# Performance work log

Hardware: AMD Instinct MI355X
Metric: run time of the kernel (lower is better)

Reference implementation:

```python
import jax, jax.numpy as jnp
import numpy as np

LN_EPS = 1e-5
ATT_EPS = 1e-6

def layer_norm(x, scale, bias):
    mu = jnp.mean(x, axis=-1, keepdims=True)
    var = jnp.mean(jnp.square(x - mu), axis=-1, keepdims=True)
    return (x - mu) * jax.lax.rsqrt(var + LN_EPS) * scale + bias

def setup_inputs() -> dict:
    key = jax.random.key(0)
    ks = jax.random.split(key, 8)
    N, C, H = 16384, 1024, 8
    s = 0.02
    return {
        "x": jax.random.normal(ks[0], (N, C), dtype=jnp.float32),
        "Wq": jax.random.normal(ks[1], (C, C), dtype=jnp.float32) * s,
        "Wkv": jax.random.normal(ks[2], (C, 2 * C), dtype=jnp.float32) * s,
        "ln1_scale": jnp.ones((C,), dtype=jnp.float32),
        "ln1_bias": jnp.zeros((C,), dtype=jnp.float32),
        "W1": jax.random.normal(ks[3], (C, C), dtype=jnp.float32) * s,
        "b1": jnp.zeros((C,), dtype=jnp.float32),
        "W2": jax.random.normal(ks[4], (C, C), dtype=jnp.float32) * s,
        "b2": jnp.zeros((C,), dtype=jnp.float32),
        "ln2_scale": jnp.ones((C,), dtype=jnp.float32),
        "ln2_bias": jnp.zeros((C,), dtype=jnp.float32),
    }

def reference(x, Wq, Wkv, ln1_scale, ln1_bias, W1, b1, W2, b2, ln2_scale, ln2_bias):
    H = 8
    N, C = x.shape
    d = C // H
    # QKV projections; torch .view(-1, d, heads) splits last dim as (d, H)
    q = (x @ Wq).reshape(N, d, H)
    kv = x @ Wkv  # [N, 2C]
    k = kv[:, :C].reshape(N, d, H)
    v = kv[:, C:].reshape(N, d, H)
    # Kernelized linear attention per head (phi = elu + 1), global segment (bi=None)
    phi_q = jax.nn.elu(q) + 1.0
    phi_k = jax.nn.elu(k) + 1.0
    kv_sum = jnp.einsum('ndh,neh->deh', phi_k, v)      # [d, d, H]
    z = jnp.sum(phi_k, axis=0)                          # [d, H]
    num = jnp.einsum('ndh,deh->neh', phi_q, kv_sum)     # [N, d, H]
    den = jnp.einsum('ndh,dh->nh', phi_q, z)            # [N, H]
    t = (num / (den[:, None, :] + ATT_EPS)).reshape(N, C)
    # AddNorm (beta=False, dropout=0): ln(t + x)
    y = layer_norm(t + x, ln1_scale, ln1_bias)
    # FFN: Linear -> GELU (exact) -> Linear
    h = jax.nn.gelu(y @ W1 + b1, approximate=False)
    f = h @ W2 + b2
    return layer_norm(f + y, ln2_scale, ln2_bias)
```

## Files before the change

kernel.cpp:

```cpp
#include <hip/hip_runtime.h>
#include <hip/hip_bf16.h>
#include <cstdint>
#include <cstddef>

typedef __bf16 bf16_t;
typedef bf16_t bf16x4 __attribute__((ext_vector_type(4)));
typedef bf16_t bf16x8 __attribute__((ext_vector_type(8)));
typedef float f32x4 __attribute__((ext_vector_type(4)));

static constexpr int NROWS = 16384;
static constexpr int CDIM  = 1024;

__device__ __forceinline__ int p6(int k) {
  return (k & 32) | ((k & 12) << 1) | ((k & 16) >> 2) | (k & 3);
}
__device__ __forceinline__ int p6i(int s) {
  return (s & 32) | ((s & 4) << 2) | ((s & 24) >> 1) | (s & 3);
}
__device__ __forceinline__ int permc(int c) {
  return (c & ~63) | p6(c & 63);
}


__device__ __forceinline__ void gload16(const bf16_t* g, bf16_t* l) {
  __builtin_amdgcn_global_load_lds((const __attribute__((address_space(1))) void*)g,
                                   (__attribute__((address_space(3))) void*)l, 16, 0, 0);
}

__device__ __forceinline__ bf16x8 ldsf128(const bf16_t* lds, int row, int ldbytes, int kbyte) {
  const char* p = (const char*)lds + row * ldbytes + (kbyte ^ ((row & 7) << 4));
  return *(const bf16x8*)p;
}

__device__ __forceinline__ float phi_fn(float v) {
  return v > 0.f ? v + 1.f : expf(v);
}
__device__ __forceinline__ float gelu_fn(float v) {
  return 0.5f * v * (1.f + erff(v * 0.70710678118654752f));
}


__global__ void cast_x_kernel(const float* __restrict__ x, bf16_t* __restrict__ xb, long nchunks) {
  long i = (long)blockIdx.x * blockDim.x + threadIdx.x;
  long stride = (long)gridDim.x * blockDim.x;
  for (long c = i; c < nchunks; c += stride) {
    long row = c >> 7;
    int p0 = (int)(c & 127) << 3;
    int group = p0 & ~63;
    int ccl = (p0 >> 3) & 7;
    int klo = ((ccl & 4) << 3) | ((ccl & 3) << 2);
    const float* src = x + row * 1024 + group + klo;
    float4 a = *(const float4*)src;
    float4 b = *(const float4*)(src + 16);
    bf16x8 o;
    o[0] = (bf16_t)a.x; o[1] = (bf16_t)a.y; o[2] = (bf16_t)a.z; o[3] = (bf16_t)a.w;
    o[4] = (bf16_t)b.x; o[5] = (bf16_t)b.y; o[6] = (bf16_t)b.z; o[7] = (bf16_t)b.w;
    *(bf16x8*)(xb + row * 1024 + p0) = o;
  }
}

__global__ void prep_w_kernel(const float* __restrict__ Wq, const float* __restrict__ Wkv,
                              const float* __restrict__ W1, const float* __restrict__ W2,
                              bf16_t* __restrict__ wqkv_bt, bf16_t* __restrict__ w1bt,
                              bf16_t* __restrict__ w2bt) {
  __shared__ float tile[64][65];
  int mode = blockIdx.z;
  const float* src; int ld; bf16_t* dst; int permute;
  if (mode == 0)      { src = Wq;          ld = 1024; dst = wqkv_bt;                       permute = 1; }
  else if (mode == 1) { src = Wkv;         ld = 2048; dst = wqkv_bt + (size_t)1024 * 1024; permute = 1; }
  else if (mode == 2) { src = Wkv + 1024;  ld = 2048; dst = wqkv_bt + (size_t)2048 * 1024; permute = 1; }
  else if (mode == 3) { src = W1;          ld = 1024; dst = w1bt;                          permute = 0; }
  else                { src = W2;          ld = 1024; dst = w2bt;                          permute = 0; }
  int r0 = blockIdx.x * 64, c0 = blockIdx.y * 64;
  int tid = threadIdx.x;
#pragma unroll
  for (int i = 0; i < 16; i++) {
    int idx = i * 256 + tid; int rr = idx >> 6, cc = idx & 63;
    tile[rr][cc] = src[(size_t)(r0 + rr) * ld + c0 + cc];
  }
  __syncthreads();
#pragma unroll
  for (int i = 0; i < 16; i++) {
    int idx = i * 256 + tid; int cc = idx >> 6, rr = idx & 63;
    int c = c0 + cc;
    int a = permute ? (((c & 7) << 7) | (c >> 3)) : c;
    dst[(size_t)a * 1024 + r0 + p6(rr)] = (bf16_t)tile[rr][cc];
  }
}


template<int MODE>
__global__ __launch_bounds__(256, 4)
void gemm_bt_kernel(const bf16_t* __restrict__ A, const bf16_t* __restrict__ Bt,
                    const float* __restrict__ bias,
                    bf16_t* __restrict__ o0, bf16_t* __restrict__ o1, bf16_t* __restrict__ o2,
                    int M, int N, int K)
{
  __shared__ bf16_t As[128 * 64];
  __shared__ bf16_t Bs[128 * 64];
  const int tid  = threadIdx.x;
  const int lane = tid & 63;
  const int wave = tid >> 6;
  const int wr = (wave >> 1) * 64, wc = (wave & 1) * 64;
  const int l15 = lane & 15, g = lane >> 4;
  const int row0 = blockIdx.x * 128, col0 = blockIdx.y * 128;
  const int cb = wave * 256;
  f32x4 acc[4][4] = {};

  for (int kt = 0; kt < K; kt += 64) {
    __syncthreads();
#pragma unroll
    for (int it = 0; it < 4; ++it) {
      int ch = cb + it * 64 + lane;
      int r = ch >> 3;
      int csrc = (ch & 7) ^ (r & 7);
      gload16(A  + (size_t)(row0 + r) * K + kt + csrc * 8, As + (size_t)(cb + it * 64) * 8);
      gload16(Bt + (size_t)(col0 + r) * K + kt + csrc * 8, Bs + (size_t)(cb + it * 64) * 8);
    }
    __syncthreads();
#pragma unroll
    for (int ks = 0; ks < 2; ++ks) {
      bf16x8 af[4], bfr[4];
#pragma unroll
      for (int i = 0; i < 4; i++) af[i]  = ldsf128(As, wr + i * 16 + l15, 128, ks * 64 + 16 * g);
#pragma unroll
      for (int i = 0; i < 4; i++) bfr[i] = ldsf128(Bs, wc + i * 16 + l15, 128, ks * 64 + 16 * g);
#pragma unroll
      for (int i = 0; i < 4; i++)
#pragma unroll
        for (int j = 0; j < 4; j++)
          acc[i][j] = __builtin_amdgcn_mfma_f32_16x16x32_bf16(af[i], bfr[j], acc[i][j], 0, 0, 0);
    }
  }

#pragma unroll
  for (int i = 0; i < 4; i++) {
    int rbase = row0 + wr + i * 16 + g * 4;
#pragma unroll
    for (int j = 0; j < 4; j++) {
      int col = col0 + wc + j * 16 + l15;
      f32x4 v = acc[i][j];
      if constexpr (MODE == 0) {
        int seg = col >> 10;
        int f   = col & 1023;
        if (seg == 0) {
          int cl = permc(f);
#pragma unroll
          for (int rr = 0; rr < 4; rr++)
            o0[(size_t)(rbase + rr) * 1024 + cl] = (bf16_t)phi_fn(v[rr]);
        } else {
          int tp = (rbase & ~63) | p6(rbase & 63);
          bf16x4 pack;
#pragma unroll
          for (int rr = 0; rr < 4; rr++)
            pack[rr] = (bf16_t)(seg == 1 ? phi_fn(v[rr]) : v[rr]);
          bf16_t* dst = (seg == 1) ? o1 : o2;
          *(bf16x4*)(dst + (size_t)f * 16384 + tp) = pack;
        }
      } else if constexpr (MODE == 1) {
        float bv = bias[col];
        int cs = permc(col);
#pragma unroll
        for (int rr = 0; rr < 4; rr++)
          o0[(size_t)(rbase + rr) * 1024 + cs] = (bf16_t)gelu_fn(v[rr] + bv);
      } else {
        float bv = bias[col];
#pragma unroll
        for (int rr = 0; rr < 4; rr++)
          o0[(size_t)(rbase + rr) * 1024 + col] = (bf16_t)(v[rr] + bv);
      }
    }
  }
}


__global__ __launch_bounds__(256, 4)
void kvsum_mfma_kernel(const bf16_t* __restrict__ phikT, const bf16_t* __restrict__ vT,
                       float* __restrict__ P, float* __restrict__ Zp)
{
  __shared__ bf16_t As[128 * 64];
  __shared__ bf16_t Bs[128 * 64];
  const int h = blockIdx.y, c = blockIdx.x;
  const bf16_t* A = phikT + (size_t)h * 128 * 16384;
  const bf16_t* B = vT    + (size_t)h * 128 * 16384;
  const int tid = threadIdx.x, lane = tid & 63, wave = tid >> 6;
  const int wr = (wave >> 1) * 64, wc = (wave & 1) * 64;
  const int l15 = lane & 15, g = lane >> 4;
  const int cb = wave * 256;
  f32x4 acc[4][4] = {};
  float zacc = 0.f;

  for (int kk = 0; kk < 4; ++kk) {
    const int kt = c * 256 + kk * 64;
    __syncthreads();
#pragma unroll
    for (int it = 0; it < 4; ++it) {
      int ch = cb + it * 64 + lane;
      int r = ch >> 3;
      int csrc = (ch & 7) ^ (r & 7);
      gload16(A + (size_t)r * 16384 + kt + csrc * 8, As + (size_t)(cb + it * 64) * 8);
      gload16(B + (size_t)r * 16384 + kt + csrc * 8, Bs + (size_t)(cb + it * 64) * 8);
    }
    __syncthreads();
    if (tid < 128) {
#pragma unroll
      for (int j = 0; j < 8; j++) {
        bf16x8 v8 = *(const bf16x8*)(As + tid * 64 + (((j + tid) & 7) * 8));
#pragma unroll
        for (int e = 0; e < 8; e++) zacc += (float)v8[e];
      }
    }
#pragma unroll
    for (int ks = 0; ks < 2; ++ks) {
      bf16x8 af[4], bfr[4];
#pragma unroll
      for (int i = 0; i < 4; i++) af[i]  = ldsf128(As, wr + i * 16 + l15, 128, ks * 64 + 16 * g);
#pragma unroll
      for (int i = 0; i < 4; i++) bfr[i] = ldsf128(Bs, wc + i * 16 + l15, 128, ks * 64 + 16 * g);
#pragma unroll
      for (int i = 0; i < 4; i++)
#pragma unroll
        for (int j = 0; j < 4; j++)
          acc[i][j] = __builtin_amdgcn_mfma_f32_16x16x32_bf16(af[i], bfr[j], acc[i][j], 0, 0, 0);
    }
  }

  float* pb = P + ((size_t)h * 64 + c) * 16384;
#pragma unroll
  for (int i = 0; i < 4; i++) {
    int e = wr + i * 16 + g * 4;
#pragma unroll
    for (int j = 0; j < 4; j++) {
      int f = wc + j * 16 + l15;
      f32x4 v = acc[i][j];
#pragma unroll
      for (int rr = 0; rr < 4; rr++)
        pb[(size_t)(e + rr) * 128 + f] = v[rr];
    }
  }
  if (tid < 128) Zp[((size_t)h * 64 + c) * 128 + tid] = zacc;
}

__global__ void reduce_kvsum_kernel(const float* __restrict__ P, const float* __restrict__ Zp,
                                    bf16_t* __restrict__ Mbt, float* __restrict__ z)
{
  int i = blockIdx.x * 256 + threadIdx.x;
  int h = i >> 14, d = (i >> 7) & 127, f = i & 127;
  const float* p = P + (size_t)h * 64 * 16384 + (size_t)d * 128 + f;
  float s = 0.f;
#pragma unroll 8
  for (int c = 0; c < 64; ++c) s += p[(size_t)c * 16384];
  int ds = (d & 64) | p6(d & 63);
  Mbt[(size_t)h * 16384 + f * 128 + ds] = (bf16_t)s;
  if (i < 1024) {
    int hh = i >> 7, dd = i & 127;
    const float* q = Zp + (size_t)hh * 64 * 128 + dd;
    float sz = 0.f;
#pragma unroll 8
    for (int c = 0; c < 64; ++c) sz += q[c * 128];
    z[i] = sz;
  }
}


__global__ __launch_bounds__(256, 3)
void attn_t_kernel(const bf16_t* __restrict__ phiq, const bf16_t* __restrict__ Mbt,
                   const float* __restrict__ z, bf16_t* __restrict__ tout)
{
  __shared__ bf16_t As[64 * 128];
  __shared__ bf16_t Bs[128 * 128];
  __shared__ float  zs[128];
  __shared__ float  dens[64];
  int h = blockIdx.y, row0 = blockIdx.x * 64;
  int tid = threadIdx.x, lane = tid & 63, wave = tid >> 6;
  int wr = (wave >> 1) * 32, wc = (wave & 1) * 64;
  int l15 = lane & 15, g = lane >> 4;

#pragma unroll
  for (int it = 0; it < 4; ++it) {
    int ch = it * 256 + tid;
    int r = ch >> 4, c8 = ch & 15;
    int cs = c8 ^ (r & 7);
    *(bf16x8*)(As + r * 128 + cs * 8) = *(const bf16x8*)(phiq + (size_t)(row0 + r) * 1024 + h * 128 + c8 * 8);
  }
#pragma unroll
  for (int it = 0; it < 8; ++it) {
    int ch = it * 256 + tid;
    int r = ch >> 4, c8 = ch & 15;
    int cs = c8 ^ (r & 7);
    *(bf16x8*)(Bs + r * 128 + cs * 8) = *(const bf16x8*)(Mbt + (size_t)h * 16384 + ch * 8);
  }
  if (tid < 128) zs[tid] = z[h * 128 + ((tid & 64) | p6i(tid & 63))];
  __syncthreads();

  f32x4 acc[2][4] = {};
#pragma unroll
  for (int ks = 0; ks < 4; ++ks) {
    bf16x8 af[2], bfr[4];
#pragma unroll
    for (int i = 0; i < 2; i++) af[i]  = ldsf128(As, wr + i * 16 + l15, 256, ks * 64 + 16 * g);
#pragma unroll
    for (int j = 0; j < 4; j++) bfr[j] = ldsf128(Bs, wc + j * 16 + l15, 256, ks * 64 + 16 * g);
#pragma unroll
    for (int i = 0; i < 2; i++)
#pragma unroll
      for (int j = 0; j < 4; j++)
        acc[i][j] = __builtin_amdgcn_mfma_f32_16x16x32_bf16(af[i], bfr[j], acc[i][j], 0, 0, 0);
  }

  if (tid < 64) {
    float s = 0.f;
    const char* p = (const char*)As + tid * 256;
    int sw = (tid & 7) << 4;
    for (int d0 = 0; d0 < 128; ++d0) {
      int d = (d0 + tid) & 127;
      bf16_t kv = *(const bf16_t*)(p + ((2 * d) ^ sw));
      s += (float)kv * zs[d];
    }
    dens[tid] = s;
  }
  __syncthreads();

#pragma unroll
  for (int i = 0; i < 2; i++) {
    int lr = wr + i * 16 + g * 4;
#pragma unroll
    for (int j = 0; j < 4; j++) {
      int col = h * 128 + wc + j * 16 + l15;
      f32x4 v = acc[i][j];
#pragma unroll
      for (int rr = 0; rr < 4; rr++) {
        float den = dens[lr + rr] + 1e-6f;
        tout[(size_t)(row0 + lr + rr) * 1024 + col] = (bf16_t)(v[rr] / den);
      }
    }
  }
}


__global__ __launch_bounds__(256, 2)
void ln1_kernel(const bf16_t* __restrict__ t, const float* __restrict__ x,
                const float* __restrict__ gma, const float* __restrict__ bta,
                bf16_t* __restrict__ y)
{
  __shared__ float s[1024];
  __shared__ float rsum[4], rsq[4];
  int n = blockIdx.x, tid = threadIdx.x;
#pragma unroll
  for (int k = 0; k < 4; k++) {
    int p = k * 256 + tid;
    float tv = (float)t[(size_t)n * 1024 + p];
    int c = ((p & 127) << 3) | (p >> 7);
    s[c] = tv;
  }
  __syncthreads();
  float sum = 0.f, sq = 0.f, sv[4];
#pragma unroll
  for (int k = 0; k < 4; k++) {
    int c = k * 256 + tid;
    float v = s[c] + x[(size_t)n * 1024 + c];
    sv[k] = v; sum += v; sq += v * v;
  }
#pragma unroll
  for (int o = 32; o > 0; o >>= 1) { sum += __shfl_down(sum, o); sq += __shfl_down(sq, o); }
  if ((tid & 63) == 0) { rsum[tid >> 6] = sum; rsq[tid >> 6] = sq; }
  __syncthreads();
  sum = rsum[0] + rsum[1] + rsum[2] + rsum[3];
  sq  = rsq[0] + rsq[1] + rsq[2] + rsq[3];
  float mu = sum * (1.f / 1024.f);
  float var = sq * (1.f / 1024.f) - mu * mu;
  float rs = rsqrtf(var + 1e-5f);
#pragma unroll
  for (int k = 0; k < 4; k++) {
    int c = k * 256 + tid;
    y[(size_t)n * 1024 + permc(c)] = (bf16_t)((sv[k] - mu) * rs * gma[c] + bta[c]);
  }
}

__global__ __launch_bounds__(256, 2)
void ln2_kernel(const bf16_t* __restrict__ f, const bf16_t* __restrict__ y,
                const float* __restrict__ gma, const float* __restrict__ bta,
                float* __restrict__ out)
{
  __shared__ float rsum[4], rsq[4];
  int n = blockIdx.x, tid = threadIdx.x;
  float sum = 0.f, sq = 0.f, sv[4];
#pragma unroll
  for (int k = 0; k < 4; k++) {
    int c = k * 256 + tid;
    float v = (float)f[(size_t)n * 1024 + c] + (float)y[(size_t)n * 1024 + permc(c)];
    sv[k] = v; sum += v; sq += v * v;
  }
#pragma unroll
  for (int o = 32; o > 0; o >>= 1) { sum += __shfl_down(sum, o); sq += __shfl_down(sq, o); }
  if ((tid & 63) == 0) { rsum[tid >> 6] = sum; rsq[tid >> 6] = sq; }
  __syncthreads();
  sum = rsum[0] + rsum[1] + rsum[2] + rsum[3];
  sq  = rsq[0] + rsq[1] + rsq[2] + rsq[3];
  float mu = sum * (1.f / 1024.f);
  float var = sq * (1.f / 1024.f) - mu * mu;
  float rs = rsqrtf(var + 1e-5f);
#pragma unroll
  for (int k = 0; k < 4; k++) {
    int c = k * 256 + tid;
    out[(size_t)n * 1024 + c] = (sv[k] - mu) * rs * gma[c] + bta[c];
  }
}


extern "C" void kernel_launch(void* const* d_in, const int* in_sizes, int n_in,
                              void* d_out, int out_size, void* d_ws, size_t ws_size,
                              hipStream_t stream)
{
  const float* x    = (const float*)d_in[0];
  const float* Wq   = (const float*)d_in[1];
  const float* Wkv  = (const float*)d_in[2];
  const float* g1   = (const float*)d_in[3];
  const float* bt1  = (const float*)d_in[4];
  const float* W1   = (const float*)d_in[5];
  const float* b1   = (const float*)d_in[6];
  const float* W2   = (const float*)d_in[7];
  const float* b2   = (const float*)d_in[8];
  const float* g2   = (const float*)d_in[9];
  const float* bt2  = (const float*)d_in[10];
  float* out = (float*)d_out;

  char* ws = (char*)d_ws;
  size_t off = 0;
  auto alloc = [&](size_t bytes) { void* p = ws + off; off += (bytes + 255) & ~(size_t)255; return p; };

  const size_t NC2 = (size_t)NROWS * CDIM * 2;
  bf16_t* xb    = (bf16_t*)alloc(NC2);
  bf16_t* wqkv  = (bf16_t*)alloc((size_t)3072 * 1024 * 2);
  bf16_t* w1bt  = (bf16_t*)alloc((size_t)1024 * 1024 * 2);
  bf16_t* w2bt  = (bf16_t*)alloc((size_t)1024 * 1024 * 2);
  bf16_t* phiq  = (bf16_t*)alloc(NC2);
  bf16_t* phikT = (bf16_t*)alloc(NC2);
  bf16_t* vT    = (bf16_t*)alloc(NC2);
  bf16_t* ybuf  = (bf16_t*)alloc(NC2);
  float*  Zp    = (float*)alloc(262144);
  float*  zbuf  = (float*)alloc(4096);
  bf16_t* Mbt   = (bf16_t*)alloc(262144);
  float*  Pbuf  = (float*)xb;
  bf16_t* tbuf  = xb;
  bf16_t* hbuf  = phikT;
  bf16_t* fbuf  = vT;

  cast_x_kernel<<<2048, 256, 0, stream>>>(x, xb, (long)NROWS * CDIM / 8);
  prep_w_kernel<<<dim3(16, 16, 5), 256, 0, stream>>>(Wq, Wkv, W1, W2, wqkv, w1bt, w2bt);

  gemm_bt_kernel<0><<<dim3(128, 24), 256, 0, stream>>>(xb, wqkv, nullptr, phiq, phikT, vT,
                                                       NROWS, 3072, 1024);
  kvsum_mfma_kernel<<<dim3(64, 8), 256, 0, stream>>>(phikT, vT, Pbuf, Zp);
  reduce_kvsum_kernel<<<512, 256, 0, stream>>>(Pbuf, Zp, Mbt, zbuf);
  attn_t_kernel<<<dim3(256, 8), 256, 0, stream>>>(phiq, Mbt, zbuf, tbuf);
  ln1_kernel<<<NROWS, 256, 0, stream>>>(tbuf, x, g1, bt1, ybuf);

  gemm_bt_kernel<1><<<dim3(128, 8), 256, 0, stream>>>(ybuf, w1bt, b1, hbuf, nullptr, nullptr,
                                                      NROWS, 1024, 1024);
  gemm_bt_kernel<2><<<dim3(128, 8), 256, 0, stream>>>(hbuf, w2bt, b2, fbuf, nullptr, nullptr,
                                                      NROWS, 1024, 1024);
  ln2_kernel<<<NROWS, 256, 0, stream>>>(fbuf, ybuf, g2, bt2, out);
}
```

Measured before the change: 313.5 us.

## Halve kvsum split count, parallelize attention denominator, read bf16 residual in LN1

The kv-sum kernel now covers 512 rows per block instead of 256, which halves the partial-sum buffer and the work in the reduction kernel. The attention denominator is computed by all 256 threads with vectorized LDS reads and a shuffle reduction, replacing 64 threads walking 128 scalar loads each. LN1 reads the residual from the bf16 copy of x instead of the fp32 input, cutting its global traffic, at some precision cost in the residual add. Buffer aliasing is reshuffled so xb stays live until LN1.

```diff
diff --git a/kernel.cpp b/kernel.cpp
--- a/kernel.cpp
+++ b/kernel.cpp
@@ -190,8 +190,8 @@
   f32x4 acc[4][4] = {};
   float zacc = 0.f;
 
-  for (int kk = 0; kk < 4; ++kk) {
-    const int kt = c * 256 + kk * 64;
+  for (int kk = 0; kk < 8; ++kk) {
+    const int kt = c * 512 + kk * 64;
     __syncthreads();
 #pragma unroll
     for (int it = 0; it < 4; ++it) {
@@ -225,7 +225,7 @@
     }
   }
 
-  float* pb = P + ((size_t)h * 64 + c) * 16384;
+  float* pb = P + ((size_t)h * 32 + c) * 16384;
 #pragma unroll
   for (int i = 0; i < 4; i++) {
     int e = wr + i * 16 + g * 4;
@@ -238,7 +238,7 @@
         pb[(size_t)(e + rr) * 128 + f] = v[rr];
     }
   }
-  if (tid < 128) Zp[((size_t)h * 64 + c) * 128 + tid] = zacc;
+  if (tid < 128) Zp[((size_t)h * 32 + c) * 128 + tid] = zacc;
 }
 
 __global__ void reduce_kvsum_kernel(const float* __restrict__ P, const float* __restrict__ Zp,
@@ -246,18 +246,18 @@
 {
   int i = blockIdx.x * 256 + threadIdx.x;
   int h = i >> 14, d = (i >> 7) & 127, f = i & 127;
-  const float* p = P + (size_t)h * 64 * 16384 + (size_t)d * 128 + f;
+  const float* p = P + (size_t)h * 32 * 16384 + (size_t)d * 128 + f;
   float s = 0.f;
 #pragma unroll 8
-  for (int c = 0; c < 64; ++c) s += p[(size_t)c * 16384];
+  for (int c = 0; c < 32; ++c) s += p[(size_t)c * 16384];
   int ds = (d & 64) | p6(d & 63);
   Mbt[(size_t)h * 16384 + f * 128 + ds] = (bf16_t)s;
   if (i < 1024) {
     int hh = i >> 7, dd = i & 127;
-    const float* q = Zp + (size_t)hh * 64 * 128 + dd;
+    const float* q = Zp + (size_t)hh * 32 * 128 + dd;
     float sz = 0.f;
 #pragma unroll 8
-    for (int c = 0; c < 64; ++c) sz += q[c * 128];
+    for (int c = 0; c < 32; ++c) sz += q[c * 128];
     z[i] = sz;
   }
 }
@@ -308,16 +308,21 @@
         acc[i][j] = __builtin_amdgcn_mfma_f32_16x16x32_bf16(af[i], bfr[j], acc[i][j], 0, 0, 0);
   }
 
-  if (tid < 64) {
+  {
+    int r = tid >> 2, q = tid & 3;
+    const char* p = (const char*)As + r * 256;
+    int sw = (r & 7) << 4;
     float s = 0.f;
-    const char* p = (const char*)As + tid * 256;
-    int sw = (tid & 7) << 4;
-    for (int d0 = 0; d0 < 128; ++d0) {
-      int d = (d0 + tid) & 127;
-      bf16_t kv = *(const bf16_t*)(p + ((2 * d) ^ sw));
-      s += (float)kv * zs[d];
-    }
-    dens[tid] = s;
+#pragma unroll
+    for (int j = 0; j < 4; j++) {
+      int gi = q * 4 + j;
+      bf16x8 v8 = *(const bf16x8*)(p + ((gi * 16) ^ sw));
+#pragma unroll
+      for (int e = 0; e < 8; e++) s += (float)v8[e] * zs[gi * 8 + e];
+    }
+    s += __shfl_xor(s, 1);
+    s += __shfl_xor(s, 2);
+    if (q == 0) dens[r] = s;
   }
   __syncthreads();
 
@@ -339,7 +344,7 @@
 
 
 __global__ __launch_bounds__(256, 2)
-void ln1_kernel(const bf16_t* __restrict__ t, const float* __restrict__ x,
+void ln1_kernel(const bf16_t* __restrict__ t, const bf16_t* __restrict__ xb,
                 const float* __restrict__ gma, const float* __restrict__ bta,
                 bf16_t* __restrict__ y)
 {
@@ -358,7 +363,7 @@
 #pragma unroll
   for (int k = 0; k < 4; k++) {
     int c = k * 256 + tid;
-    float v = s[c] + x[(size_t)n * 1024 + c];
+    float v = s[c] + (float)xb[(size_t)n * 1024 + permc(c)];
     sv[k] = v; sum += v; sq += v * v;
   }
 #pragma unroll
@@ -441,8 +446,8 @@
   float*  Zp    = (float*)alloc(262144);
   float*  zbuf  = (float*)alloc(4096);
   bf16_t* Mbt   = (bf16_t*)alloc(262144);
-  float*  Pbuf  = (float*)xb;
-  bf16_t* tbuf  = xb;
+  float*  Pbuf  = (float*)ybuf;
+  bf16_t* tbuf  = phikT;
   bf16_t* hbuf  = phikT;
   bf16_t* fbuf  = vT;
 
@@ -451,10 +456,10 @@
 
   gemm_bt_kernel<0><<<dim3(128, 24), 256, 0, stream>>>(xb, wqkv, nullptr, phiq, phikT, vT,
                                                        NROWS, 3072, 1024);
-  kvsum_mfma_kernel<<<dim3(64, 8), 256, 0, stream>>>(phikT, vT, Pbuf, Zp);
+  kvsum_mfma_kernel<<<dim3(32, 8), 256, 0, stream>>>(phikT, vT, Pbuf, Zp);
   reduce_kvsum_kernel<<<512, 256, 0, stream>>>(Pbuf, Zp, Mbt, zbuf);
   attn_t_kernel<<<dim3(256, 8), 256, 0, stream>>>(phiq, Mbt, zbuf, tbuf);
-  ln1_kernel<<<NROWS, 256, 0, stream>>>(tbuf, x, g1, bt1, ybuf);
+  ln1_kernel<<<NROWS, 256, 0, stream>>>(tbuf, xb, g1, bt1, ybuf);
 
   gemm_bt_kernel<1><<<dim3(128, 8), 256, 0, stream>>>(ybuf, w1bt, b1, hbuf, nullptr, nullptr,
                                                       NROWS, 1024, 1024);
```

New measurement: 310.0 us (median of 2 runs). About the same (-1.1%).
